# Kernel tuning notes

Measured on AMD Instinct MI355X. Metric: run time of the kernel, lower is better.

## Reference

```python
import jax, jax.numpy as jnp
import numpy as np

B, NPTS = 16, 10000
COORD_DIM, PARAM_DIM = 3, 6   # coords are 3-d, sdf adds 1 channel -> trunk input dim 4
HID, L, OUT = 128, 4, 5


def rowdy(x, a, w):
    # Rowdy activation: base tanh plus learnable per-feature sinusoidal perturbation
    return jnp.tanh(x) + a * jnp.sin(w * x)


def setup_inputs() -> dict:
    key = jax.random.key(0)
    ks = jax.random.split(key, 16)
    s = lambda i, shape, sc=1.0: jax.random.normal(ks[i], shape, dtype=jnp.float32) * sc
    return {
        "coords": s(0, (B, NPTS, COORD_DIM)),
        "sdf":    s(1, (B, NPTS, 1)),
        "params": s(2, (B, PARAM_DIM)),
        # branch MLP params
        "Wb0": s(3, (PARAM_DIM, HID), 0.3), "bb0": jnp.zeros((HID,), jnp.float32),
        "Wb":  s(4, (L - 1, HID, HID), 0.08), "bb": jnp.zeros((L - 1, HID), jnp.float32),
        "Wbf": s(5, (HID, HID * OUT), 0.08), "bbf": jnp.zeros((HID * OUT,), jnp.float32),
        "ab":  s(6, (L, HID), 0.1), "wb": jnp.ones((L, HID), jnp.float32),
        # trunk params (layer 0 has input dim COORD_DIM+1 from cat(coords, sdf))
        "Wt0": s(7, (COORD_DIM + 1, HID), 0.3), "bt0": jnp.zeros((HID,), jnp.float32),
        "Wt":  s(8, (L - 1, HID, HID), 0.08), "bt": jnp.zeros((L - 1, HID), jnp.float32),
        "Wtf": s(9, (HID, HID), 0.08), "btf": jnp.zeros((HID,), jnp.float32),
        "at":  s(10, (L, HID), 0.1), "wt": jnp.ones((L, HID), jnp.float32),
    }


def reference(coords, sdf, params, Wb0, bb0, Wb, bb, Wbf, bbf, ab, wb,
              Wt0, bt0, Wt, bt, Wtf, btf, at, wt):
    # ---- branch MLP with per-layer hidden outputs ----
    h = rowdy(params @ Wb0 + bb0, ab[0], wb[0])        # (B, HID)
    hiddens = [h]
    for i in range(L - 1):
        h = rowdy(h @ Wb[i] + bb[i], ab[i + 1], wb[i + 1])
        hiddens.append(h)
    branch_out = h @ Wbf + bbf                         # (B, HID*OUT)

    # ---- fusion gates: running sums of branch hiddens ----
    gate = [hiddens[0]]
    for i in range(1, L):
        gate.append(hiddens[i] + gate[-1])

    # ---- trunk: Linear -> Rowdy -> gate multiply (dropout p=0 is identity) ----
    x = jnp.concatenate([coords, sdf], axis=-1)        # (B, NPTS, 4)
    x = rowdy(x @ Wt0 + bt0, at[0], wt[0]) * gate[0][:, None, :]
    for i in range(L - 1):
        x = rowdy(x @ Wt[i] + bt[i], at[i + 1], wt[i + 1]) * gate[i + 1][:, None, :]
    trunk = x @ Wtf + btf                              # (B, NPTS, HID)

    # ---- final contraction: batched GEMM instead of broadcast-mul + sum ----
    bc = branch_out.reshape(B, OUT, HID)               # (B, OUT, HID)
    return jnp.einsum('bph,boh->bpo', trunk, bc)       # (B, NPTS, OUT)
```

## Files before the change

### kernel.cpp

```cpp
#include <hip/hip_runtime.h>
#include <hip/hip_bf16.h>
#include <math.h>

#define BATCH 16
#define NPTS 10000
#define HID 128
#define NOUT 5
#define TM 64
#define TPB 256

typedef unsigned short ushort_t;
typedef __attribute__((ext_vector_type(8))) short short8;
typedef __attribute__((ext_vector_type(4))) float f32x4;

__device__ __forceinline__ float fast_tanh(float x) {
    float e = __expf(2.0f * x);
    return 1.0f - 2.0f * __builtin_amdgcn_rcpf(e + 1.0f);
}
__device__ __forceinline__ float rowdy_act(float x, float a, float w) {
    return fast_tanh(x) + a * __sinf(w * x);
}
__device__ __forceinline__ ushort_t f32_to_bf16_rn(float f) {
    unsigned u = __float_as_uint(f);
    unsigned r = (u + 0x7FFFu + ((u >> 16) & 1u)) >> 16;
    return (ushort_t)r;
}
__device__ __forceinline__ float bf16_to_f32(ushort_t u) {
    return __uint_as_float(((unsigned)u) << 16);
}

__global__ __launch_bounds__(256) void prep_branch_kernel(
    const float* __restrict__ Wt, ushort_t* __restrict__ whi, ushort_t* __restrict__ wlo,
    const float* __restrict__ params, const float* __restrict__ Wb0, const float* __restrict__ bb0,
    const float* __restrict__ Wb, const float* __restrict__ bbv,
    const float* __restrict__ Wbf, const float* __restrict__ bbf,
    const float* __restrict__ ab, const float* __restrict__ wb,
    const float* __restrict__ Wtf, const float* __restrict__ btf,
    float* __restrict__ g_gates, float* __restrict__ g_wcomb, float* __restrict__ g_bcomb)
{
    __shared__ __align__(16) float wsh[HID * HID];
    __shared__ __align__(16) float hbuf[HID];
    __shared__ __align__(16) float pred[8 * HID];
    __shared__ __align__(16) float bcbuf[NOUT * HID];
    __shared__ __align__(16) float wcred[2 * NOUT * HID];

    const int tid = threadIdx.x;

    if (blockIdx.x < 3) {
        const int l = blockIdx.x;
        const float4* src = (const float4*)(Wt + l * HID * HID);
        #pragma unroll
        for (int i = 0; i < 16; i++)
            ((float4*)wsh)[i * 256 + tid] = src[i * 256 + tid];
        __syncthreads();
        for (int e = tid; e < 2048; e += 256) {
            int t = e >> 8, s = (e >> 6) & 3, lam = e & 63;
            int k0 = s * 32 + (lam >> 4) * 8;
            int n = t * 16 + (lam & 15);
            short8 h8, l8;
            #pragma unroll
            for (int j = 0; j < 8; j++) {
                float v = wsh[(k0 + j) * HID + n];
                ushort_t h = f32_to_bf16_rn(v);
                float rem = v - bf16_to_f32(h);
                h8[j] = (short)h;
                l8[j] = (short)f32_to_bf16_rn(rem);
            }
            ((short8*)whi)[l * 2048 + e] = h8;
            ((short8*)wlo)[l * 2048 + e] = l8;
        }
        return;
    }

    const int b = blockIdx.x - 3;
    const int j = tid & 127;
    const bool act = (tid < 128);
    const int jg = tid & 31;
    const int ks = tid >> 5;

    {
        float z = bb0[j];
        #pragma unroll
        for (int k = 0; k < 6; k++) z += params[b * 6 + k] * Wb0[k * HID + j];
        float h = rowdy_act(z, ab[j], wb[j]);
        if (act) {
            g_gates[b * 4 * HID + j] = h;
            hbuf[j] = h;
        }
    }
    __syncthreads();

    float g = 0.f;
    if (act) g = hbuf[j];

    for (int i = 0; i < 3; i++) {
        const float4* W4 = (const float4*)(Wb + i * HID * HID);
        float4 acc = make_float4(0.f, 0.f, 0.f, 0.f);
        #pragma unroll
        for (int kk = 0; kk < 16; kk++) {
            int k = ks * 16 + kk;
            float4 wv = W4[k * 32 + jg];
            float hv = hbuf[k];
            acc.x += hv * wv.x;
            acc.y += hv * wv.y;
            acc.z += hv * wv.z;
            acc.w += hv * wv.w;
        }
        *(float4*)&pred[ks * HID + 4 * jg] = acc;
        __syncthreads();
        float hn = 0.f;
        if (act) {
            float zz = bbv[i * HID + j];
            #pragma unroll
            for (int s = 0; s < 8; s++) zz += pred[s * HID + j];
            hn = rowdy_act(zz, ab[(i + 1) * HID + j], wb[(i + 1) * HID + j]);
            g += hn;
            g_gates[b * 4 * HID + (i + 1) * HID + j] = g;
        }
        __syncthreads();
        if (act) hbuf[j] = hn;
        __syncthreads();
    }

    for (int o = 0; o < NOUT; o++) {
        const float4* W4 = (const float4*)Wbf;
        float4 acc = make_float4(0.f, 0.f, 0.f, 0.f);
        #pragma unroll
        for (int kk = 0; kk < 16; kk++) {
            int k = ks * 16 + kk;
            float4 wv = W4[k * 160 + o * 32 + jg];
            float hv = hbuf[k];
            acc.x += hv * wv.x;
            acc.y += hv * wv.y;
            acc.z += hv * wv.z;
            acc.w += hv * wv.w;
        }
        *(float4*)&pred[ks * HID + 4 * jg] = acc;
        __syncthreads();
        if (act) {
            float s = bbf[o * HID + j];
            #pragma unroll
            for (int sI = 0; sI < 8; sI++) s += pred[sI * HID + j];
            bcbuf[o * HID + j] = s;
        }
        __syncthreads();
    }

    {
        const int jj = tid & 127;
        const int hs = tid >> 7;
        const float4* Wtf4 = (const float4*)Wtf;
        float wc[NOUT] = {0.f, 0.f, 0.f, 0.f, 0.f};
        #pragma unroll
        for (int h4 = 0; h4 < 16; h4++) {
            float4 wv = Wtf4[jj * 32 + hs * 16 + h4];
            int h2 = hs * 64 + h4 * 4;
            #pragma unroll
            for (int o = 0; o < NOUT; o++) {
                float4 bv = *(const float4*)&bcbuf[o * HID + h2];
                wc[o] += wv.x * bv.x + wv.y * bv.y + wv.z * bv.z + wv.w * bv.w;
            }
        }
        #pragma unroll
        for (int o = 0; o < NOUT; o++) wcred[(hs * NOUT + o) * HID + jj] = wc[o];
        __syncthreads();
        if (act) {
            #pragma unroll
            for (int o = 0; o < NOUT; o++)
                g_wcomb[b * HID * NOUT + jj * NOUT + o] =
                    wcred[o * HID + jj] + wcred[(NOUT + o) * HID + jj];
        }
        if (tid < NOUT) {
            float acc = 0.f;
            for (int h2 = 0; h2 < HID; h2++) acc += btf[h2] * bcbuf[tid * HID + h2];
            g_bcomb[b * NOUT + tid] = acc;
        }
    }
}

__global__ __launch_bounds__(TPB, 3) void trunk_kernel(
    const float* __restrict__ coords, const float* __restrict__ sdf,
    const float* __restrict__ Wt0, const float* __restrict__ bt0,
    const float* __restrict__ bt, const float* __restrict__ at, const float* __restrict__ wt,
    const float* __restrict__ g_gates, const float* __restrict__ g_wcomb,
    const float* __restrict__ g_bcomb,
    const ushort_t* __restrict__ whi, const ushort_t* __restrict__ wlo,
    float* __restrict__ out)
{
    __shared__ __align__(16) ushort_t xfh[TM * HID];
    __shared__ __align__(16) ushort_t xfl[TM * HID];
    __shared__ __align__(16) float sb_bias[4][HID];
    __shared__ __align__(16) float sb_a[4][HID];
    __shared__ __align__(16) float sb_w[4][HID];
    __shared__ __align__(16) float sb_g[4][HID];
    __shared__ __align__(16) float Wt0s[4][HID];
    __shared__ __align__(16) float Wc[NOUT][HID];
    __shared__ float bcs[NOUT];
    __shared__ __align__(16) float xin[TM][4];
    __shared__ float redbuf[4][TM][NOUT];

    const int b = blockIdx.y;
    const int p0 = blockIdx.x * TM;
    const int tid = threadIdx.x;
    const int w = tid >> 6;
    const int lam = tid & 63;
    const int quad = lam >> 4, lq = lam & 15;

    for (int idx = tid; idx < 4 * HID; idx += TPB) {
        int l = idx >> 7, jj = idx & (HID - 1);
        sb_bias[l][jj] = (l == 0) ? bt0[jj] : bt[(l - 1) * HID + jj];
        sb_a[l][jj] = at[idx];
        sb_w[l][jj] = wt[idx];
        sb_g[l][jj] = g_gates[b * 4 * HID + idx];
        Wt0s[l][jj] = Wt0[idx];
    }
    for (int idx = tid; idx < HID * NOUT; idx += TPB) {
        int k = idx / NOUT, o = idx - k * NOUT;
        Wc[o][k] = g_wcomb[b * HID * NOUT + idx];
    }
    if (tid < NOUT) bcs[tid] = g_bcomb[b * NOUT + tid];

    if (tid < 192) {
        int p = tid / 3, c = tid - p * 3;
        int gp = p0 + p;
        xin[p][c] = (gp < NPTS) ? coords[(size_t)(b * NPTS + gp) * 3 + c] : 0.0f;
    } else {
        int p = tid - 192;
        int gp = p0 + p;
        xin[p][3] = (gp < NPTS) ? sdf[b * NPTS + gp] : 0.0f;
    }
    __syncthreads();

    {
        const int s = w;
        float w0c[8], w1c[8], w2c[8], w3c[8], bc8[8], ac[8], wc8[8], gc[8];
        #pragma unroll
        for (int jj = 0; jj < 8; jj++) {
            int col = s * 32 + quad * 8 + jj;
            w0c[jj] = Wt0s[0][col];
            w1c[jj] = Wt0s[1][col];
            w2c[jj] = Wt0s[2][col];
            w3c[jj] = Wt0s[3][col];
            bc8[jj] = sb_bias[0][col];
            ac[jj] = sb_a[0][col];
            wc8[jj] = sb_w[0][col];
            gc[jj] = sb_g[0][col];
        }
        #pragma unroll
        for (int mt = 0; mt < 4; mt++) {
            int row = mt * 16 + lq;
            float4 xi = *(const float4*)&xin[row][0];
            float y[8];
            #pragma unroll
            for (int jj = 0; jj < 8; jj++) {
                float zv = xi.x * w0c[jj] + xi.y * w1c[jj] + xi.z * w2c[jj] + xi.w * w3c[jj] + bc8[jj];
                y[jj] = rowdy_act(zv, ac[jj], wc8[jj]) * gc[jj];
            }
            uint4 hp, lp;
            unsigned* hpp = (unsigned*)&hp;
            unsigned* lpp = (unsigned*)&lp;
            #pragma unroll
            for (int pr = 0; pr < 4; pr++) {
                unsigned ue = __float_as_uint(y[2 * pr]);
                unsigned uo = __float_as_uint(y[2 * pr + 1]);
                hpp[pr] = (ue >> 16) | (uo & 0xFFFF0000u);
                float le = y[2 * pr] - __uint_as_float(ue & 0xFFFF0000u);
                float lo_ = y[2 * pr + 1] - __uint_as_float(uo & 0xFFFF0000u);
                lpp[pr] = (__float_as_uint(le) >> 16) | (__float_as_uint(lo_) & 0xFFFF0000u);
            }
            *(uint4*)&xfh[((mt * 4 + s) * 64 + lam) * 8] = hp;
            *(uint4*)&xfl[((mt * 4 + s) * 64 + lam) * 8] = lp;
        }
    }
    __syncthreads();

    const short8* Wh8 = (const short8*)whi;
    const short8* Wl8 = (const short8*)wlo;
    const int lq3 = lq >> 3;
    const int jlow = lq & 7;
    const int ebase0 = w * 512 + (lq3 * 16 + quad * 4) * 8 + jlow;
    const int ebase1 = w * 512 + ((2 + lq3) * 16 + quad * 4) * 8 + jlow;
    const int n0 = 32 * w + lq, n1 = 32 * w + 16 + lq;

    for (int l = 1; l <= 3; l++) {
        const int fb = (l - 1) * 32;
        float b0 = sb_bias[l][n0], b1 = sb_bias[l][n1];
        f32x4 acc[4][2];
        #pragma unroll
        for (int mt = 0; mt < 4; mt++) {
            acc[mt][0] = (f32x4){b0, b0, b0, b0};
            acc[mt][1] = (f32x4){b1, b1, b1, b1};
        }
        for (int s = 0; s < 4; s++) {
            short8 bh0 = Wh8[(size_t)(fb + (2 * w) * 4 + s) * 64 + lam];
            short8 bl0 = Wl8[(size_t)(fb + (2 * w) * 4 + s) * 64 + lam];
            short8 bh1 = Wh8[(size_t)(fb + (2 * w + 1) * 4 + s) * 64 + lam];
            short8 bl1 = Wl8[(size_t)(fb + (2 * w + 1) * 4 + s) * 64 + lam];
            #pragma unroll
            for (int mt = 0; mt < 4; mt++) {
                short8 ah = *(const short8*)&xfh[((mt * 4 + s) * 64 + lam) * 8];
                short8 al = *(const short8*)&xfl[((mt * 4 + s) * 64 + lam) * 8];
                acc[mt][0] = __builtin_amdgcn_mfma_f32_16x16x32_bf16(ah, bh0, acc[mt][0], 0, 0, 0);
                acc[mt][0] = __builtin_amdgcn_mfma_f32_16x16x32_bf16(al, bh0, acc[mt][0], 0, 0, 0);
                acc[mt][0] = __builtin_amdgcn_mfma_f32_16x16x32_bf16(ah, bl0, acc[mt][0], 0, 0, 0);
                acc[mt][1] = __builtin_amdgcn_mfma_f32_16x16x32_bf16(ah, bh1, acc[mt][1], 0, 0, 0);
                acc[mt][1] = __builtin_amdgcn_mfma_f32_16x16x32_bf16(al, bh1, acc[mt][1], 0, 0, 0);
                acc[mt][1] = __builtin_amdgcn_mfma_f32_16x16x32_bf16(ah, bl1, acc[mt][1], 0, 0, 0);
            }
        }
        __syncthreads();
        float a0 = sb_a[l][n0], ww0 = sb_w[l][n0], gg0 = sb_g[l][n0];
        float a1 = sb_a[l][n1], ww1 = sb_w[l][n1], gg1 = sb_g[l][n1];
        #pragma unroll
        for (int mt = 0; mt < 4; mt++) {
            #pragma unroll
            for (int r = 0; r < 4; r++) {
                float y0 = rowdy_act(acc[mt][0][r], a0, ww0) * gg0;
                float y1 = rowdy_act(acc[mt][1][r], a1, ww1) * gg1;
                unsigned u0 = __float_as_uint(y0);
                unsigned u1 = __float_as_uint(y1);
                float l0f = y0 - __uint_as_float(u0 & 0xFFFF0000u);
                float l1f = y1 - __uint_as_float(u1 & 0xFFFF0000u);
                xfh[mt * 2048 + ebase0 + r * 8] = (ushort_t)(u0 >> 16);
                xfl[mt * 2048 + ebase0 + r * 8] = (ushort_t)(__float_as_uint(l0f) >> 16);
                xfh[mt * 2048 + ebase1 + r * 8] = (ushort_t)(u1 >> 16);
                xfl[mt * 2048 + ebase1 + r * 8] = (ushort_t)(__float_as_uint(l1f) >> 16);
            }
        }
        __syncthreads();
    }

    {
        int q = tid & 3, p = tid >> 2;
        int mt = p >> 4, prow = p & 15;
        float part[NOUT] = {0.f, 0.f, 0.f, 0.f, 0.f};
        #pragma unroll
        for (int g8 = 0; g8 < 4; g8++) {
            int base = ((mt * 4 + q) * 64 + g8 * 16 + prow) * 8;
            uint4 h4 = *(const uint4*)&xfh[base];
            uint4 l4 = *(const uint4*)&xfl[base];
            const unsigned* hu = (const unsigned*)&h4;
            const unsigned* lu = (const unsigned*)&l4;
            int c0 = q * 32 + g8 * 8;
            float xv[8];
            #pragma unroll
            for (int pr = 0; pr < 4; pr++) {
                xv[2 * pr]     = __uint_as_float(hu[pr] << 16) + __uint_as_float(lu[pr] << 16);
                xv[2 * pr + 1] = __uint_as_float(hu[pr] & 0xFFFF0000u) + __uint_as_float(lu[pr] & 0xFFFF0000u);
            }
            #pragma unroll
            for (int o = 0; o < NOUT; o++) {
                float4 wa = *(const float4*)&Wc[o][c0];
                float4 wb4 = *(const float4*)&Wc[o][c0 + 4];
                part[o] += xv[0] * wa.x + xv[1] * wa.y + xv[2] * wa.z + xv[3] * wa.w
                         + xv[4] * wb4.x + xv[5] * wb4.y + xv[6] * wb4.z + xv[7] * wb4.w;
            }
        }
        #pragma unroll
        for (int o = 0; o < NOUT; o++) redbuf[q][p][o] = part[o];
    }
    __syncthreads();
    if (tid < TM) {
        int gp = p0 + tid;
        if (gp < NPTS) {
            #pragma unroll
            for (int o = 0; o < NOUT; o++) {
                float s = bcs[o] + redbuf[0][tid][o] + redbuf[1][tid][o]
                                 + redbuf[2][tid][o] + redbuf[3][tid][o];
                out[(size_t)(b * NPTS + gp) * NOUT + o] = s;
            }
        }
    }
}

extern "C" void kernel_launch(void* const* d_in, const int* in_sizes, int n_in,
                              void* d_out, int out_size, void* d_ws, size_t ws_size,
                              hipStream_t stream) {
    (void)in_sizes; (void)n_in; (void)out_size; (void)ws_size;
    const float* coords = (const float*)d_in[0];
    const float* sdf    = (const float*)d_in[1];
    const float* params = (const float*)d_in[2];
    const float* Wb0    = (const float*)d_in[3];
    const float* bb0    = (const float*)d_in[4];
    const float* Wb     = (const float*)d_in[5];
    const float* bbv    = (const float*)d_in[6];
    const float* Wbf    = (const float*)d_in[7];
    const float* bbf    = (const float*)d_in[8];
    const float* ab     = (const float*)d_in[9];
    const float* wb     = (const float*)d_in[10];
    const float* Wt0    = (const float*)d_in[11];
    const float* bt0    = (const float*)d_in[12];
    const float* Wt     = (const float*)d_in[13];
    const float* bt     = (const float*)d_in[14];
    const float* Wtf    = (const float*)d_in[15];
    const float* btf    = (const float*)d_in[16];
    const float* at     = (const float*)d_in[17];
    const float* wt     = (const float*)d_in[18];
    float* out = (float*)d_out;
    float* ws  = (float*)d_ws;

    float* g_gates = ws;
    float* g_wcomb = ws + 8192;
    float* g_bcomb = ws + 8192 + 10240;
    ushort_t* whi = (ushort_t*)(ws + 18512);
    ushort_t* wlo = whi + 3 * HID * HID;

    hipLaunchKernelGGL(prep_branch_kernel, dim3(19), dim3(256), 0, stream,
                       Wt, whi, wlo,
                       params, Wb0, bb0, Wb, bbv, Wbf, bbf, ab, wb, Wtf, btf,
                       g_gates, g_wcomb, g_bcomb);

    dim3 grid((NPTS + TM - 1) / TM, BATCH);
    hipLaunchKernelGGL(trunk_kernel, grid, dim3(TPB), 0, stream,
                       coords, sdf, Wt0, bt0, bt, at, wt,
                       g_gates, g_wcomb, g_bcomb, whi, wlo, out);
}
```

Before: 183.2 us.

## Swizzle trunk LDS activation layout and prefetch branch weights into registers

```diff
diff --git a/kernel.cpp b/kernel.cpp
--- a/kernel.cpp
+++ b/kernel.cpp
@@ -29,7 +29,10 @@
     return __uint_as_float(((unsigned)u) << 16);
 }
 
-__global__ __launch_bounds__(256) void prep_branch_kernel(
+__device__ __forceinline__ int swzv(int v) { return v ^ ((v >> 3) & 3); }
+__device__ __forceinline__ int swzs(int s) { return s ^ ((s >> 3) & 0x18); }
+
+__global__ __launch_bounds__(256, 1) void prep_branch_kernel(
     const float* __restrict__ Wt, ushort_t* __restrict__ whi, ushort_t* __restrict__ wlo,
     const float* __restrict__ params, const float* __restrict__ Wb0, const float* __restrict__ bb0,
     const float* __restrict__ Wb, const float* __restrict__ bbv,
@@ -43,6 +46,8 @@
     __shared__ __align__(16) float pred[8 * HID];
     __shared__ __align__(16) float bcbuf[NOUT * HID];
     __shared__ __align__(16) float wcred[2 * NOUT * HID];
+    __shared__ __align__(16) float btfs[HID];
+    __shared__ float bred[NOUT][2];
 
     const int tid = threadIdx.x;
 
@@ -77,88 +82,118 @@
     const bool act = (tid < 128);
     const int jg = tid & 31;
     const int ks = tid >> 5;
-
-    {
-        float z = bb0[j];
-        #pragma unroll
-        for (int k = 0; k < 6; k++) z += params[b * 6 + k] * Wb0[k * HID + j];
-        float h = rowdy_act(z, ab[j], wb[j]);
-        if (act) {
-            g_gates[b * 4 * HID + j] = h;
-            hbuf[j] = h;
-        }
+    const int wv = tid >> 6;
+
+    float abr[4], wbr[4];
+    #pragma unroll
+    for (int l = 0; l < 4; l++) { abr[l] = ab[l * HID + j]; wbr[l] = wb[l * HID + j]; }
+    float bb0r = bb0[j];
+    float bbvr[3];
+    #pragma unroll
+    for (int i = 0; i < 3; i++) bbvr[i] = bbv[i * HID + j];
+    float bbfr[NOUT];
+    #pragma unroll
+    for (int o = 0; o < NOUT; o++) bbfr[o] = bbf[o * HID + j];
+    float p6[6], w0r[6];
+    #pragma unroll
+    for (int k = 0; k < 6; k++) { p6[k] = params[b * 6 + k]; w0r[k] = Wb0[k * HID + j]; }
+    if (act) btfs[j] = btf[j];
+
+    float4 A[16], Bv[16];
+    {
+        const float4* W4 = (const float4*)Wb;
+        #pragma unroll
+        for (int kk = 0; kk < 16; kk++) A[kk] = W4[(ks * 16 + kk) * 32 + jg];
+    }
+
+    float g;
+    {
+        float z = bb0r;
+        #pragma unroll
+        for (int k = 0; k < 6; k++) z += p6[k] * w0r[k];
+        float h = rowdy_act(z, abr[0], wbr[0]);
+        if (act) { g_gates[b * 4 * HID + j] = h; hbuf[j] = h; }
+        g = h;
     }
     __syncthreads();
 
-    float g = 0.f;
-    if (act) g = hbuf[j];
-
-    for (int i = 0; i < 3; i++) {
-        const float4* W4 = (const float4*)(Wb + i * HID * HID);
-        float4 acc = make_float4(0.f, 0.f, 0.f, 0.f);
-        #pragma unroll
-        for (int kk = 0; kk < 16; kk++) {
-            int k = ks * 16 + kk;
-            float4 wv = W4[k * 32 + jg];
-            float hv = hbuf[k];
-            acc.x += hv * wv.x;
-            acc.y += hv * wv.y;
-            acc.z += hv * wv.z;
-            acc.w += hv * wv.w;
-        }
-        *(float4*)&pred[ks * HID + 4 * jg] = acc;
-        __syncthreads();
-        float hn = 0.f;
-        if (act) {
-            float zz = bbv[i * HID + j];
-            #pragma unroll
-            for (int s = 0; s < 8; s++) zz += pred[s * HID + j];
-            hn = rowdy_act(zz, ab[(i + 1) * HID + j], wb[(i + 1) * HID + j]);
-            g += hn;
-            g_gates[b * 4 * HID + (i + 1) * HID + j] = g;
-        }
-        __syncthreads();
-        if (act) hbuf[j] = hn;
-        __syncthreads();
-    }
-
-    for (int o = 0; o < NOUT; o++) {
-        const float4* W4 = (const float4*)Wbf;
-        float4 acc = make_float4(0.f, 0.f, 0.f, 0.f);
-        #pragma unroll
-        for (int kk = 0; kk < 16; kk++) {
-            int k = ks * 16 + kk;
-            float4 wv = W4[k * 160 + o * 32 + jg];
-            float hv = hbuf[k];
-            acc.x += hv * wv.x;
-            acc.y += hv * wv.y;
-            acc.z += hv * wv.z;
-            acc.w += hv * wv.w;
-        }
-        *(float4*)&pred[ks * HID + 4 * jg] = acc;
-        __syncthreads();
-        if (act) {
-            float s = bbf[o * HID + j];
-            #pragma unroll
-            for (int sI = 0; sI < 8; sI++) s += pred[sI * HID + j];
-            bcbuf[o * HID + j] = s;
-        }
-        __syncthreads();
-    }
-
-    {
-        const int jj = tid & 127;
-        const int hs = tid >> 7;
+#define BR_LAYER(CUR, I) { \
+        float4 acc = make_float4(0.f, 0.f, 0.f, 0.f); \
+        _Pragma("unroll") \
+        for (int kk = 0; kk < 16; kk++) { \
+            float hv = hbuf[ks * 16 + kk]; \
+            acc.x += hv * CUR[kk].x; acc.y += hv * CUR[kk].y; \
+            acc.z += hv * CUR[kk].z; acc.w += hv * CUR[kk].w; \
+        } \
+        *(float4*)&pred[ks * HID + 4 * jg] = acc; \
+        __syncthreads(); \
+        if (act) { \
+            float zz = bbvr[I]; \
+            _Pragma("unroll") \
+            for (int s = 0; s < 8; s++) zz += pred[s * HID + j]; \
+            float hn = rowdy_act(zz, abr[(I) + 1], wbr[(I) + 1]); \
+            g += hn; \
+            g_gates[b * 4 * HID + ((I) + 1) * HID + j] = g; \
+            hbuf[j] = hn; \
+        } \
+        __syncthreads(); }
+
+#define BR_CHUNK(CUR, O) { \
+        float4 acc = make_float4(0.f, 0.f, 0.f, 0.f); \
+        _Pragma("unroll") \
+        for (int kk = 0; kk < 16; kk++) { \
+            float hv = hbuf[ks * 16 + kk]; \
+            acc.x += hv * CUR[kk].x; acc.y += hv * CUR[kk].y; \
+            acc.z += hv * CUR[kk].z; acc.w += hv * CUR[kk].w; \
+        } \
+        *(float4*)&pred[ks * HID + 4 * jg] = acc; \
+        __syncthreads(); \
+        if (act) { \
+            float s = bbfr[O]; \
+            _Pragma("unroll") \
+            for (int sI = 0; sI < 8; sI++) s += pred[sI * HID + j]; \
+            bcbuf[(O) * HID + j] = s; \
+            float pp = btfs[j] * s; \
+            _Pragma("unroll") \
+            for (int off = 32; off >= 1; off >>= 1) pp += __shfl_xor(pp, off, 64); \
+            if ((tid & 63) == 0) bred[O][wv] = pp; \
+        } \
+        __syncthreads(); }
+
+#define PF_WB(DST, I) { const float4* W4 = (const float4*)(Wb + (I) * HID * HID); \
+        _Pragma("unroll") \
+        for (int kk = 0; kk < 16; kk++) DST[kk] = W4[(ks * 16 + kk) * 32 + jg]; }
+#define PF_BF(DST, O) { const float4* W4 = (const float4*)Wbf; \
+        _Pragma("unroll") \
+        for (int kk = 0; kk < 16; kk++) DST[kk] = W4[(ks * 16 + kk) * 160 + (O) * 32 + jg]; }
+
+    PF_WB(Bv, 1)  BR_LAYER(A, 0)
+    PF_WB(A, 2)   BR_LAYER(Bv, 1)
+    PF_BF(Bv, 0)  BR_LAYER(A, 2)
+
+    PF_BF(A, 1)   BR_CHUNK(Bv, 0)
+    PF_BF(Bv, 2)  BR_CHUNK(A, 1)
+    PF_BF(A, 3)   BR_CHUNK(Bv, 2)
+    PF_BF(Bv, 4)  BR_CHUNK(A, 3)
+    const int jj = tid & 127;
+    const int hs = tid >> 7;
+    {
         const float4* Wtf4 = (const float4*)Wtf;
+        #pragma unroll
+        for (int kk = 0; kk < 16; kk++) A[kk] = Wtf4[jj * 32 + hs * 16 + kk];
+    }
+    BR_CHUNK(Bv, 4)
+
+    {
         float wc[NOUT] = {0.f, 0.f, 0.f, 0.f, 0.f};
         #pragma unroll
         for (int h4 = 0; h4 < 16; h4++) {
-            float4 wv = Wtf4[jj * 32 + hs * 16 + h4];
+            float4 wvv = A[h4];
             int h2 = hs * 64 + h4 * 4;
             #pragma unroll
             for (int o = 0; o < NOUT; o++) {
                 float4 bv = *(const float4*)&bcbuf[o * HID + h2];
-                wc[o] += wv.x * bv.x + wv.y * bv.y + wv.z * bv.z + wv.w * bv.w;
+                wc[o] += wvv.x * bv.x + wvv.y * bv.y + wvv.z * bv.z + wvv.w * bv.w;
             }
         }
         #pragma unroll
@@ -170,12 +205,12 @@
                 g_wcomb[b * HID * NOUT + jj * NOUT + o] =
                     wcred[o * HID + jj] + wcred[(NOUT + o) * HID + jj];
         }
-        if (tid < NOUT) {
-            float acc = 0.f;
-            for (int h2 = 0; h2 < HID; h2++) acc += btf[h2] * bcbuf[tid * HID + h2];
-            g_bcomb[b * NOUT + tid] = acc;
-        }
-    }
+        if (tid < NOUT) g_bcomb[b * NOUT + tid] = bred[tid][0] + bred[tid][1];
+    }
+#undef BR_LAYER
+#undef BR_CHUNK
+#undef PF_WB
+#undef PF_BF
 }
 
 __global__ __launch_bounds__(TPB, 3) void trunk_kernel(
@@ -268,8 +303,9 @@
                 float lo_ = y[2 * pr + 1] - __uint_as_float(uo & 0xFFFF0000u);
                 lpp[pr] = (__float_as_uint(le) >> 16) | (__float_as_uint(lo_) & 0xFFFF0000u);
             }
-            *(uint4*)&xfh[((mt * 4 + s) * 64 + lam) * 8] = hp;
-            *(uint4*)&xfl[((mt * 4 + s) * 64 + lam) * 8] = lp;
+            int vdst = swzv((mt * 4 + s) * 64 + lam) * 8;
+            *(uint4*)&xfh[vdst] = hp;
+            *(uint4*)&xfl[vdst] = lp;
         }
     }
     __syncthreads();
@@ -298,8 +334,9 @@
             short8 bl1 = Wl8[(size_t)(fb + (2 * w + 1) * 4 + s) * 64 + lam];
             #pragma unroll
             for (int mt = 0; mt < 4; mt++) {
-                short8 ah = *(const short8*)&xfh[((mt * 4 + s) * 64 + lam) * 8];
-                short8 al = *(const short8*)&xfl[((mt * 4 + s) * 64 + lam) * 8];
+                int vsrc = swzv((mt * 4 + s) * 64 + lam) * 8;
+                short8 ah = *(const short8*)&xfh[vsrc];
+                short8 al = *(const short8*)&xfl[vsrc];
                 acc[mt][0] = __builtin_amdgcn_mfma_f32_16x16x32_bf16(ah, bh0, acc[mt][0], 0, 0, 0);
                 acc[mt][0] = __builtin_amdgcn_mfma_f32_16x16x32_bf16(al, bh0, acc[mt][0], 0, 0, 0);
                 acc[mt][0] = __builtin_amdgcn_mfma_f32_16x16x32_bf16(ah, bl0, acc[mt][0], 0, 0, 0);
@@ -321,10 +358,12 @@
                 unsigned u1 = __float_as_uint(y1);
                 float l0f = y0 - __uint_as_float(u0 & 0xFFFF0000u);
                 float l1f = y1 - __uint_as_float(u1 & 0xFFFF0000u);
-                xfh[mt * 2048 + ebase0 + r * 8] = (ushort_t)(u0 >> 16);
-                xfl[mt * 2048 + ebase0 + r * 8] = (ushort_t)(__float_as_uint(l0f) >> 16);
-                xfh[mt * 2048 + ebase1 + r * 8] = (ushort_t)(u1 >> 16);
-                xfl[mt * 2048 + ebase1 + r * 8] = (ushort_t)(__float_as_uint(l1f) >> 16);
+                int i0 = swzs(mt * 2048 + ebase0 + r * 8);
+                int i1 = swzs(mt * 2048 + ebase1 + r * 8);
+                xfh[i0] = (ushort_t)(u0 >> 16);
+                xfl[i0] = (ushort_t)(__float_as_uint(l0f) >> 16);
+                xfh[i1] = (ushort_t)(u1 >> 16);
+                xfl[i1] = (ushort_t)(__float_as_uint(l1f) >> 16);
             }
         }
         __syncthreads();
@@ -336,7 +375,7 @@
         float part[NOUT] = {0.f, 0.f, 0.f, 0.f, 0.f};
         #pragma unroll
         for (int g8 = 0; g8 < 4; g8++) {
-            int base = ((mt * 4 + q) * 64 + g8 * 16 + prow) * 8;
+            int base = swzv((mt * 4 + q) * 64 + g8 * 16 + prow) * 8;
             uint4 h4 = *(const uint4*)&xfh[base];
             uint4 l4 = *(const uint4*)&xfl[base];
             const unsigned* hu = (const unsigned*)&h4;
```

New measurement: 176.1 us. -3.9%, faster.
